# Optimization experiments

Measured on AMD Instinct MI355X. Metric: run time of the kernel, lower is better.

Reference implementation:

```python
import jax, jax.numpy as jnp
import numpy as np

EXPAND = 1
N_CHUNKS = 6
CHUNK = 4

def setup_inputs() -> dict:
    key = jax.random.key(0)
    k1, k2 = jax.random.split(key)
    B = 4_000_000
    pre = jax.random.normal(k1, (B, 25), dtype=jnp.float32)
    tar = jax.random.uniform(k2, (B, 25), dtype=jnp.float32)
    return {"pre": pre, "tar": tar}

def reference(pre, tar):
    B = pre.shape[0]
    # 6 chunks of 4: softmax over each chunk, scaled by 3*expand.
    chunks = pre[:, :N_CHUNKS * CHUNK].reshape(B, N_CHUNKS, CHUNK)
    out24 = 3.0 * EXPAND * jax.nn.softmax(chunks, axis=-1)  # [B,6,4]
    tar24 = tar[:, :N_CHUNKS * CHUNK].reshape(B, N_CHUNKS, CHUNK)
    # out[24] = relu(pre[24]) is computed in the original but never enters the
    # loss (loss uses out[0:24] only), so it is omitted.
    per_sample = jnp.mean(jnp.abs(out24 - tar24), axis=(1, 2))  # mean over 24 elems
    return jnp.sum(per_sample)
```

## Files before the change

### kernel.cpp

```cpp
#include <hip/hip_runtime.h>

#define THREADS 256
#define ROWS_PER_BLOCK 256
#define ROW 25
#define TILE_FLOATS (ROWS_PER_BLOCK * ROW)
#define TILE_VEC4 (TILE_FLOATS / 4)
#define FULL_K (TILE_VEC4 / THREADS)
#define MAX_BLOCKS 1536

__device__ __forceinline__ void load16_to_lds(const float* g, float* l) {
    __builtin_amdgcn_global_load_lds(
        (const __attribute__((address_space(1))) void*)g,
        (__attribute__((address_space(3))) void*)l,
        16, 0, 0);
}

__launch_bounds__(THREADS, 6)
__global__ void loss_soft_add_kernel(const float* __restrict__ pre,
                                     const float* __restrict__ tar,
                                     float* __restrict__ out, int B) {
    __shared__ __attribute__((aligned(16))) float s_pre[TILE_FLOATS];
    __shared__ float s_part[THREADS / 64];

    const int tid = threadIdx.x;
    const int ntiles = (B + ROWS_PER_BLOCK - 1) / ROWS_PER_BLOCK;

    float acc = 0.0f;

    for (int t = blockIdx.x; t < ntiles; t += gridDim.x) {
        const int row0 = t * ROWS_PER_BLOCK;
        const int nrows = min(ROWS_PER_BLOCK, B - row0);
        const int nfloats = nrows * ROW;
        const size_t base = (size_t)row0 * ROW;

        __syncthreads();

        if (nfloats == TILE_FLOATS) {
            const float* gp = pre + base;
            #pragma unroll
            for (int k = 0; k < FULL_K; ++k) {
                const int idx = tid + k * THREADS;
                load16_to_lds(gp + idx * 4, &s_pre[idx * 4]);
            }
            if (tid < TILE_VEC4 - FULL_K * THREADS) {
                const int idx = tid + FULL_K * THREADS;
                load16_to_lds(gp + idx * 4, &s_pre[idx * 4]);
            }
        } else {
            for (int idx = tid; idx < nfloats; idx += THREADS)
                s_pre[idx] = pre[base + idx];
        }
        __syncthreads();

        if (tid < nrows) {
            float* rp = &s_pre[tid * ROW];
            #pragma unroll
            for (int c = 0; c < 6; ++c) {
                const float x0 = rp[c * 4 + 0];
                const float x1 = rp[c * 4 + 1];
                const float x2 = rp[c * 4 + 2];
                const float x3 = rp[c * 4 + 3];
                const float m = fmaxf(fmaxf(x0, x1), fmaxf(x2, x3));
                const float e0 = __expf(x0 - m);
                const float e1 = __expf(x1 - m);
                const float e2 = __expf(x2 - m);
                const float e3 = __expf(x3 - m);
                const float k3 = 3.0f / (e0 + e1 + e2 + e3);
                rp[c * 4 + 0] = e0 * k3;
                rp[c * 4 + 1] = e1 * k3;
                rp[c * 4 + 2] = e2 * k3;
                rp[c * 4 + 3] = e3 * k3;
            }
        }
        __syncthreads();

        if (nfloats == TILE_FLOATS) {
            const float4* st = (const float4*)(tar + base);
            const float4* so = (const float4*)s_pre;
            #pragma unroll
            for (int k = 0; k <= FULL_K; ++k) {
                const int idx = tid + k * THREADS;
                if (idx < TILE_VEC4) {
                    const float4 tv = st[idx];
                    const float4 ov = so[idx];
                    unsigned col = (unsigned)(idx * 4) % 25u;
                    acc += (col == 24u) ? 0.0f : fabsf(ov.x - tv.x); col = (col == 24u) ? 0u : col + 1u;
                    acc += (col == 24u) ? 0.0f : fabsf(ov.y - tv.y); col = (col == 24u) ? 0u : col + 1u;
                    acc += (col == 24u) ? 0.0f : fabsf(ov.z - tv.z); col = (col == 24u) ? 0u : col + 1u;
                    acc += (col == 24u) ? 0.0f : fabsf(ov.w - tv.w);
                }
            }
        } else {
            for (int i = tid; i < nfloats; i += THREADS) {
                if ((unsigned)i % 25u != 24u)
                    acc += fabsf(s_pre[i] - tar[base + i]);
            }
        }
    }

    acc *= (1.0f / 24.0f);

    #pragma unroll
    for (int off = 32; off > 0; off >>= 1)
        acc += __shfl_down(acc, off, 64);
    const int wid = tid >> 6, lane = tid & 63;
    if (lane == 0) s_part[wid] = acc;
    __syncthreads();
    if (tid == 0) {
        const float bsum = s_part[0] + s_part[1] + s_part[2] + s_part[3];
        atomicAdd(out, bsum);
    }
}

extern "C" void kernel_launch(void* const* d_in, const int* in_sizes, int n_in,
                              void* d_out, int out_size, void* d_ws, size_t ws_size,
                              hipStream_t stream) {
    const float* pre = (const float*)d_in[0];
    const float* tar = (const float*)d_in[1];
    float* out = (float*)d_out;
    const int B = in_sizes[0] / ROW;

    hipMemsetAsync(d_out, 0, sizeof(float) * out_size, stream);

    const int ntiles = (B + ROWS_PER_BLOCK - 1) / ROWS_PER_BLOCK;
    const int blocks = ntiles < MAX_BLOCKS ? ntiles : MAX_BLOCKS;
    loss_soft_add_kernel<<<blocks, THREADS, 0, stream>>>(pre, tar, out, B);
}
```

Baseline: 724.9 us.

## Stage target tile in LDS and fuse softmax with abs-diff accumulation

Loads the target tile into LDS alongside the prediction tile using async global-to-LDS copies. The softmax is then fused with the L1 accumulation per row, which removes the write-back of softmax results, one barrier, and the separate vectorized pass with modulo column masking. Doubling LDS per block cuts occupancy, so the grid cap and launch-bounds occupancy hint are halved to match. Row-strided LDS reads of the target (stride 25) may hit some bank conflicts, and fewer resident blocks means fewer loads in flight.

```diff
diff --git a/kernel.cpp b/kernel.cpp
--- a/kernel.cpp
+++ b/kernel.cpp
@@ -6,7 +6,7 @@
 #define TILE_FLOATS (ROWS_PER_BLOCK * ROW)
 #define TILE_VEC4 (TILE_FLOATS / 4)
 #define FULL_K (TILE_VEC4 / THREADS)
-#define MAX_BLOCKS 1536
+#define MAX_BLOCKS 768
 
 __device__ __forceinline__ void load16_to_lds(const float* g, float* l) {
     __builtin_amdgcn_global_load_lds(
@@ -15,11 +15,12 @@
         16, 0, 0);
 }
 
-__launch_bounds__(THREADS, 6)
+__launch_bounds__(THREADS, 3)
 __global__ void loss_soft_add_kernel(const float* __restrict__ pre,
                                      const float* __restrict__ tar,
                                      float* __restrict__ out, int B) {
     __shared__ __attribute__((aligned(16))) float s_pre[TILE_FLOATS];
+    __shared__ __attribute__((aligned(16))) float s_tar[TILE_FLOATS];
     __shared__ float s_part[THREADS / 64];
 
     const int tid = threadIdx.x;
@@ -37,23 +38,30 @@
 
         if (nfloats == TILE_FLOATS) {
             const float* gp = pre + base;
+            const float* gt = tar + base;
             #pragma unroll
             for (int k = 0; k < FULL_K; ++k) {
                 const int idx = tid + k * THREADS;
                 load16_to_lds(gp + idx * 4, &s_pre[idx * 4]);
+                load16_to_lds(gt + idx * 4, &s_tar[idx * 4]);
             }
             if (tid < TILE_VEC4 - FULL_K * THREADS) {
                 const int idx = tid + FULL_K * THREADS;
                 load16_to_lds(gp + idx * 4, &s_pre[idx * 4]);
+                load16_to_lds(gt + idx * 4, &s_tar[idx * 4]);
             }
         } else {
-            for (int idx = tid; idx < nfloats; idx += THREADS)
+            for (int idx = tid; idx < nfloats; idx += THREADS) {
                 s_pre[idx] = pre[base + idx];
+                s_tar[idx] = tar[base + idx];
+            }
         }
         __syncthreads();
 
         if (tid < nrows) {
-            float* rp = &s_pre[tid * ROW];
+            const float* rp = &s_pre[tid * ROW];
+            const float* rt = &s_tar[tid * ROW];
+            float total = 0.0f;
             #pragma unroll
             for (int c = 0; c < 6; ++c) {
                 const float x0 = rp[c * 4 + 0];
@@ -66,35 +74,12 @@
                 const float e2 = __expf(x2 - m);
                 const float e3 = __expf(x3 - m);
                 const float k3 = 3.0f / (e0 + e1 + e2 + e3);
-                rp[c * 4 + 0] = e0 * k3;
-                rp[c * 4 + 1] = e1 * k3;
-                rp[c * 4 + 2] = e2 * k3;
-                rp[c * 4 + 3] = e3 * k3;
+                total += fabsf(e0 * k3 - rt[c * 4 + 0]);
+                total += fabsf(e1 * k3 - rt[c * 4 + 1]);
+                total += fabsf(e2 * k3 - rt[c * 4 + 2]);
+                total += fabsf(e3 * k3 - rt[c * 4 + 3]);
             }
-        }
-        __syncthreads();
-
-        if (nfloats == TILE_FLOATS) {
-            const float4* st = (const float4*)(tar + base);
-            const float4* so = (const float4*)s_pre;
-            #pragma unroll
-            for (int k = 0; k <= FULL_K; ++k) {
-                const int idx = tid + k * THREADS;
-                if (idx < TILE_VEC4) {
-                    const float4 tv = st[idx];
-                    const float4 ov = so[idx];
-                    unsigned col = (unsigned)(idx * 4) % 25u;
-                    acc += (col == 24u) ? 0.0f : fabsf(ov.x - tv.x); col = (col == 24u) ? 0u : col + 1u;
-                    acc += (col == 24u) ? 0.0f : fabsf(ov.y - tv.y); col = (col == 24u) ? 0u : col + 1u;
-                    acc += (col == 24u) ? 0.0f : fabsf(ov.z - tv.z); col = (col == 24u) ? 0u : col + 1u;
-                    acc += (col == 24u) ? 0.0f : fabsf(ov.w - tv.w);
-                }
-            }
-        } else {
-            for (int i = tid; i < nfloats; i += THREADS) {
-                if ((unsigned)i % 25u != 24u)
-                    acc += fabsf(s_pre[i] - tar[base + i]);
-            }
+            acc += total;
         }
     }
 
```

Measured after the change: 736.1 us. Within noise of the previous version (+1.6%).
